# Kernel tuning notes

Hardware: AMD Instinct MI355X
Metric: run time of the kernel (lower is better)

Reference implementation:

```python
import jax, jax.numpy as jnp
import numpy as np

B = 4096
D = 512
N_I = 1000000
N_T = 1000000
GAMMA = 0.8
EPS = 1e-10
RHO_I = 8.0
RHO_T = 8.0
ETA_INIT = 1e-05
BETA_U = 0.5
GRAD_CLIP = 5.0
TAU_MIN, TAU_MAX = 0.005, 0.05
TAU_INIT = 0.01


def setup_inputs() -> dict:
    key = jax.random.key(0)
    k1, k2 = jax.random.split(key)
    img = jax.random.normal(k1, (B, D), jnp.float32)
    txt = jax.random.normal(k2, (B, D), jnp.float32)
    # CLIP-style L2-normalized features
    img = img / jnp.linalg.norm(img, axis=1, keepdims=True)
    txt = txt / jnp.linalg.norm(txt, axis=1, keepdims=True)
    return {
        "image_features": img,
        "text_features": txt,
        "s_I": jnp.zeros(N_I, jnp.float32),
        "s_T": jnp.zeros(N_T, jnp.float32),
        "b_I": jnp.zeros(N_I, jnp.float32),
        "b_T": jnp.zeros(N_T, jnp.float32),
        "u_I": jnp.zeros(N_I, jnp.float32),
        "u_T": jnp.zeros(N_T, jnp.float32),
        "tau_I": jnp.full((N_I,), TAU_INIT, jnp.float32),
        "tau_T": jnp.full((N_T,), TAU_INIT, jnp.float32),
        "image_ids": jnp.arange(B, dtype=jnp.int32),
        "text_ids": jnp.arange(B, dtype=jnp.int32),
        "epoch": 1,
    }


def reference(image_features, text_features, s_I, s_T, b_I, b_T, u_I, u_T,
              tau_I, tau_T, image_ids, text_ids, epoch):
    sg = jax.lax.stop_gradient
    sim = jnp.einsum('id,jd->ij', image_features, text_features)  # [B,B]
    diag = jnp.diagonal(sim)
    Bn = sim.shape[0]
    tau_img = tau_I[image_ids]  # [B]
    tau_txt = tau_T[text_ids]   # [B]
    image_diffs = sim - diag[:, None]
    text_diffs = sim - diag[None, :]
    # .detach() in the original -> stop_gradient here
    idt = sg(image_diffs / tau_img[:, None])
    tdt = sg(text_diffs / tau_txt[None, :])
    old_b_I = b_I[image_ids]
    old_b_T = b_T[text_ids]
    # running max for log-sum-exp stabilization
    b_I_row = jnp.maximum(idt.max(axis=1), old_b_I)
    b_T_col = jnp.maximum(tdt.max(axis=0), old_b_T)
    b_I_new = b_I.at[image_ids].set(b_I_row)
    b_T_new = b_T.at[text_ids].set(b_T_col)
    mask = 1.0 - jnp.eye(Bn, dtype=sim.dtype)
    exp_i = jnp.exp(idt - b_I_row[:, None]) * mask
    exp_t = jnp.exp(tdt - b_T_col[None, :]) * mask
    g_I = exp_i.sum(axis=1)
    g_T = exp_t.sum(axis=0)
    if epoch == 0:
        sI = g_I
        sT = g_T
    else:
        sI = (1.0 - GAMMA) * s_I[image_ids] * jnp.exp(old_b_I - b_I_row) + GAMMA * g_I
        sT = (1.0 - GAMMA) * s_T[text_ids] * jnp.exp(old_b_T - b_T_col) + GAMMA * g_T
    s_I_new = s_I.at[image_ids].set(sI)
    s_T_new = s_T.at[text_ids].set(sT)
    w_i = sg(exp_i / (sI[:, None] + EPS))
    w_t = sg(exp_t / (sT[None, :] + EPS))
    image_loss = (w_i * image_diffs).sum(axis=1)
    text_loss = (w_t * text_diffs).sum(axis=0)
    total_loss = image_loss.mean() + text_loss.mean()
    tw_i = jnp.log(sI / (Bn - 1)) + b_I_row + RHO_I - (w_i * idt).sum(axis=1)
    tw_t = jnp.log(sT / (Bn - 1)) + b_T_col + RHO_T - (w_t * tdt).sum(axis=0)
    # torch uses in-place clamp_ on a view, so the returned means are clipped
    tw_i = jnp.clip(tw_i, -GRAD_CLIP, GRAD_CLIP)
    tw_t = jnp.clip(tw_t, -GRAD_CLIP, GRAD_CLIP)
    u_I_val = (1.0 - BETA_U) * u_I[image_ids] + BETA_U * tw_i
    u_T_val = (1.0 - BETA_U) * u_T[text_ids] + BETA_U * tw_t
    u_I_new = u_I.at[image_ids].set(u_I_val)
    u_T_new = u_T.at[text_ids].set(u_T_val)
    tau_I_new = tau_I.at[image_ids].set(jnp.clip(tau_img - ETA_INIT * u_I_val, TAU_MIN, TAU_MAX))
    tau_T_new = tau_T.at[text_ids].set(jnp.clip(tau_txt - ETA_INIT * u_T_val, TAU_MIN, TAU_MAX))
    return (total_loss, tau_img.mean(), tau_txt.mean(), tw_i.mean(), tw_t.mean(),
            s_I_new, s_T_new, b_I_new, b_T_new, u_I_new, u_T_new, tau_I_new, tau_T_new)
```

## Files before the change

kernel.cpp:

```cpp
#include <hip/hip_runtime.h>

typedef unsigned short u16;
typedef unsigned int u32;

typedef __bf16 bf16x8 __attribute__((ext_vector_type(8)));
typedef float floatx4 __attribute__((ext_vector_type(4)));

__device__ __forceinline__ u16 f2bf(float f) {
    union { float f; u32 u; } c; c.f = f;
    u32 u = c.u;
    u32 r = u + 0x7FFFu + ((u >> 16) & 1u);
    return (u16)(r >> 16);
}
__device__ __forceinline__ float bf2f(u16 x) {
    union { u32 u; float f; } c; c.u = ((u32)x) << 16; return c.f;
}

__device__ __forceinline__ void comb(float& M, float& P0, float& P1,
                                     float m, float p0, float p1) {
    float nm = fmaxf(M, m);
    float s = __expf(M - nm), t = __expf(m - nm);
    P0 = P0 * s + p0 * t;
    P1 = P1 * s + p1 * t;
    M = nm;
}

__device__ __forceinline__ void gload16(const void* g, void* l) {
    __builtin_amdgcn_global_load_lds(
        (const __attribute__((address_space(1))) void*)g,
        (__attribute__((address_space(3))) void*)l, 16, 0, 0);
}

__global__ __launch_bounds__(256) void presplit(
    const float* __restrict__ a, const float* __restrict__ b,
    u16* __restrict__ Ah, u16* __restrict__ Al,
    u16* __restrict__ Bh, u16* __restrict__ Bl, int n,
    const float* __restrict__ tauI, const float* __restrict__ tauT,
    const int* __restrict__ img_ids, const int* __restrict__ txt_ids,
    float* __restrict__ taur, float* __restrict__ tauc) {
    if (blockIdx.y == 0 && blockIdx.x < 16) {
        int t = blockIdx.x * 256 + threadIdx.x;
        taur[t] = tauI[img_ids[t]];
        tauc[t] = tauT[txt_ids[t]];
    }
    const float* src = blockIdx.y ? b : a;
    u16* dh = blockIdx.y ? Bh : Ah;
    u16* dl = blockIdx.y ? Bl : Al;
    int i = (blockIdx.x * 256 + threadIdx.x) * 8;
    if (i >= n) return;
    float4 v0 = *(const float4*)&src[i];
    float4 v1 = *(const float4*)&src[i + 4];
    float xs[8] = {v0.x, v0.y, v0.z, v0.w, v1.x, v1.y, v1.z, v1.w};
    u16 h[8], l[8];
#pragma unroll
    for (int e = 0; e < 8; e++) {
        h[e] = f2bf(xs[e]);
        l[e] = f2bf(xs[e] - bf2f(h[e]));
    }
    int r = i >> 9, k = i & 511;
    int off = (((r >> 4) << 4) + (k >> 5)) * 512 + ((((k >> 3) & 3) << 4) + (r & 15)) * 8;
    *(uint4*)&dh[off] = *(uint4*)h;
    *(uint4*)&dl[off] = *(uint4*)l;
}

__global__ __launch_bounds__(512, 2) void gemm_flash(
    const u16* __restrict__ Ah, const u16* __restrict__ Al,
    const u16* __restrict__ Bh, const u16* __restrict__ Bl,
    const float* __restrict__ taur, const float* __restrict__ tauc,
    float* __restrict__ rowpart, float* __restrict__ colpart,
    float* __restrict__ diag,
    const float* __restrict__ p0, const float* __restrict__ p1,
    const float* __restrict__ p2, const float* __restrict__ p3,
    const float* __restrict__ p4, const float* __restrict__ p5,
    const float* __restrict__ p6, const float* __restrict__ p7,
    float* __restrict__ out, long long n) {
    __shared__ u16 tiles[65536];

    const int bid  = blockIdx.x;
    const int tid  = threadIdx.x;
    const int wave = tid >> 6, lane = tid & 63;
    const int lr = lane & 15, quad = lane >> 4;
    const int waveM = wave >> 2, waveN = wave & 3;
    const int x = bid & 7, s = bid >> 3;
    const int rowtile = (x >> 2) * 8 + (s >> 2);
    const int coltile = (x & 3) * 4 + (s & 3);
    const int rowBase = rowtile * 256;
    const int colBase = coltile * 256;

    const int sa = wave >> 1;
    const u16* gb = (sa == 0) ? Ah : (sa == 1) ? Al : (sa == 2) ? Bh : Bl;
    const int base16 = ((sa < 2) ? rowBase : colBase) >> 4;
    const int jb = (wave & 1) * 8;

#define STAGE(slice, bufb)                                                    \
    {                                                                         \
        _Pragma("unroll")                                                     \
        for (int j = 0; j < 8; j++) {                                         \
            size_t ge = ((size_t)(base16 + jb + j)) * 8192 +                  \
                        (size_t)(slice) * 512 + lane * 8;                     \
            gload16(gb + ge, &tiles[(bufb) + (wave * 8 + j) * 512]);          \
        }                                                                     \
    }

    floatx4 acc[8][4];
#pragma unroll
    for (int mi = 0; mi < 8; mi++)
#pragma unroll
        for (int ni = 0; ni < 4; ni++) acc[mi][ni] = (floatx4)0.0f;

    const int Gq = (int)((n - 3) >> 2);
    const int ni32 = (int)n;
    float* dst5 = out + 5;

    STAGE(0, 0)

    if (bid == 0 && tid < 32) {
        int arr = tid >> 2, j = tid & 3;
        const float* sp = (arr & 4) ? ((arr & 2) ? ((arr & 1) ? p7 : p6) : ((arr & 1) ? p5 : p4))
                                    : ((arr & 2) ? ((arr & 1) ? p3 : p2) : ((arr & 1) ? p1 : p0));
        float* dp = dst5 + (size_t)arr * (size_t)n;
        long long tail0 = 3 + 4 * (long long)Gq;
        if (j < 3) dp[j] = sp[j];
        else
            for (long long z = tail0; z < n; z++) dp[z] = sp[z];
    }
    __syncthreads();

#pragma unroll 1
    for (int t = 0; t < 16; t++) {
        const int cb = (t & 1) << 15;
        const int nb = cb ^ 32768;
        if (t < 15) STAGE(t + 1, nb)

        bool docopy = false;
        float c0 = 0.f, c1 = 0.f, c2 = 0.f, c3 = 0.f;
        int cdst = 0;
        {
            int c = bid * 512 + tid + t * 131072;
            int ck = c >> 18;
            int g = c & 262143;
            if (g < Gq) {
                docopy = true;
                int ce = 3 + 4 * g;
                cdst = ck * ni32 + ce;
                const float* sp = (ck & 4) ? ((ck & 2) ? ((ck & 1) ? p7 : p6) : ((ck & 1) ? p5 : p4))
                                           : ((ck & 2) ? ((ck & 1) ? p3 : p2) : ((ck & 1) ? p1 : p0));
                c0 = sp[ce]; c1 = sp[ce + 1]; c2 = sp[ce + 2]; c3 = sp[ce + 3];
            }
        }

        {
            const int ab = cb + lane * 8;
            bf16x8 bh[4], bl[4];
#pragma unroll
            for (int ni = 0; ni < 4; ni++) {
                bh[ni] = *(const bf16x8*)&tiles[ab + (32 + waveN * 4 + ni) * 512];
                bl[ni] = *(const bf16x8*)&tiles[ab + (48 + waveN * 4 + ni) * 512];
            }
#pragma unroll
            for (int mi = 0; mi < 8; mi++) {
                bf16x8 ah = *(const bf16x8*)&tiles[ab + (waveM * 8 + mi) * 512];
                bf16x8 al = *(const bf16x8*)&tiles[ab + (16 + waveM * 8 + mi) * 512];
#pragma unroll
                for (int ni = 0; ni < 4; ni++) {
                    acc[mi][ni] = __builtin_amdgcn_mfma_f32_16x16x32_bf16(ah, bh[ni], acc[mi][ni], 0, 0, 0);
                    acc[mi][ni] = __builtin_amdgcn_mfma_f32_16x16x32_bf16(ah, bl[ni], acc[mi][ni], 0, 0, 0);
                    acc[mi][ni] = __builtin_amdgcn_mfma_f32_16x16x32_bf16(al, bh[ni], acc[mi][ni], 0, 0, 0);
                }
            }
        }

        if (docopy) {
            float4 q = {c0, c1, c2, c3};
            *(float4*)&dst5[cdst] = q;
        }
        __syncthreads();
    }
#undef STAGE

    float* redbuf = (float*)tiles;

    if (rowtile == coltile) {
#pragma unroll
        for (int mi = 0; mi < 8; mi++)
#pragma unroll
            for (int ni = 0; ni < 4; ni++) {
                if (waveM * 128 + mi * 16 != waveN * 64 + ni * 16) continue;
#pragma unroll
                for (int r = 0; r < 4; r++)
                    if (lr == quad * 4 + r)
                        diag[colBase + waveN * 64 + ni * 16 + lr] = acc[mi][ni][r];
            }
    }

#pragma unroll
    for (int mi = 0; mi < 8; mi++) {
#pragma unroll
        for (int r = 0; r < 4; r++) {
            int row_local = waveM * 128 + mi * 16 + quad * 4 + r;
            float vmax = fmaxf(fmaxf(acc[mi][0][r], acc[mi][1][r]),
                               fmaxf(acc[mi][2][r], acc[mi][3][r]));
#pragma unroll
            for (int mask = 1; mask <= 8; mask <<= 1)
                vmax = fmaxf(vmax, __shfl_xor(vmax, mask));
            float it = 1.0f / taur[rowBase + row_local];
            float M = vmax * it;
            float P0 = 0.f, P1 = 0.f;
#pragma unroll
            for (int ni = 0; ni < 4; ni++) {
                float y = acc[mi][ni][r] * it;
                float e = __expf(y - M);
                P0 += e;
                P1 += y * e;
            }
#pragma unroll
            for (int mask = 1; mask <= 8; mask <<= 1) {
                P0 += __shfl_xor(P0, mask);
                P1 += __shfl_xor(P1, mask);
            }
            if (lr == 0) {
                int xx = (row_local * 4 + waveN) * 3;
                redbuf[xx] = M; redbuf[xx + 1] = P0; redbuf[xx + 2] = P1;
            }
        }
    }

#pragma unroll
    for (int ni = 0; ni < 4; ni++) {
        int col_local = waveN * 64 + ni * 16 + lr;
        float vmax = -3.4e38f;
#pragma unroll
        for (int mi = 0; mi < 8; mi++)
            vmax = fmaxf(vmax,
                fmaxf(fmaxf(acc[mi][ni][0], acc[mi][ni][1]),
                      fmaxf(acc[mi][ni][2], acc[mi][ni][3])));
#pragma unroll
        for (int mask = 16; mask <= 32; mask <<= 1)
            vmax = fmaxf(vmax, __shfl_xor(vmax, mask));
        float it = 1.0f / tauc[colBase + col_local];
        float M = vmax * it;
        float P0 = 0.f, P1 = 0.f;
#pragma unroll
        for (int mi = 0; mi < 8; mi++)
#pragma unroll
            for (int r = 0; r < 4; r++) {
                float y = acc[mi][ni][r] * it;
                float e = __expf(y - M);
                P0 += e;
                P1 += y * e;
            }
#pragma unroll
        for (int mask = 16; mask <= 32; mask <<= 1) {
            P0 += __shfl_xor(P0, mask);
            P1 += __shfl_xor(P1, mask);
        }
        if (quad == 0) {
            int xx = 3072 + (col_local * 2 + waveM) * 3;
            redbuf[xx] = M; redbuf[xx + 1] = P0; redbuf[xx + 2] = P1;
        }
    }
    __syncthreads();

    if (tid < 256) {
        int xx = tid * 12;
        float M = redbuf[xx], P0 = redbuf[xx + 1], P1 = redbuf[xx + 2];
        comb(M, P0, P1, redbuf[xx + 3], redbuf[xx + 4], redbuf[xx + 5]);
        comb(M, P0, P1, redbuf[xx + 6], redbuf[xx + 7], redbuf[xx + 8]);
        comb(M, P0, P1, redbuf[xx + 9], redbuf[xx + 10], redbuf[xx + 11]);
        float* dst = &rowpart[(size_t)(rowBase + tid) * 48 + coltile * 3];
        dst[0] = M; dst[1] = P0; dst[2] = P1;
    } else {
        int c = tid - 256;
        int xx = 3072 + c * 6;
        float M = redbuf[xx], P0 = redbuf[xx + 1], P1 = redbuf[xx + 2];
        comb(M, P0, P1, redbuf[xx + 3], redbuf[xx + 4], redbuf[xx + 5]);
        float* dst = &colpart[(size_t)(colBase + c) * 48 + rowtile * 3];
        dst[0] = M; dst[1] = P0; dst[2] = P1;
    }
}

struct FinArgs {
    const float* rowpart; const float* colpart; const float* diag;
    const float* tauI; const float* sI; const float* bI; const float* uI;
    const float* tauT; const float* sT; const float* bT; const float* uT;
    const int* img_ids; const int* txt_ids; const int* epoch_p;
    float* out; float* rowbuf; long long n;
};

__global__ __launch_bounds__(256) void rows_final(FinArgs a) {
    int t = blockIdx.x * 256 + threadIdx.x;
    int side = t >> 12, i = t & 4095;
    const float* part   = side ? a.colpart : a.rowpart;
    const int*   ids    = side ? a.txt_ids : a.img_ids;
    const float* tau_in = side ? a.tauT : a.tauI;
    const float* s_in   = side ? a.sT   : a.sI;
    const float* b_in   = side ? a.bT   : a.bI;
    const float* u_in   = side ? a.uT   : a.uI;

    const int id = ids[i];
    const float dg = a.diag[i];

    const float4* p4 = (const float4*)(part + (size_t)i * 48);
    float v[48];
#pragma unroll
    for (int k = 0; k < 12; k++) {
        float4 q = p4[k];
        v[4 * k]     = q.x;
        v[4 * k + 1] = q.y;
        v[4 * k + 2] = q.z;
        v[4 * k + 3] = q.w;
    }
    float M = -3.4e38f, P0 = 0.f, P1 = 0.f;
#pragma unroll
    for (int k = 0; k < 16; k++)
        comb(M, P0, P1, v[3 * k], v[3 * k + 1], v[3 * k + 2]);

    const float tau   = tau_in[id];
    const float old_b = b_in[id];
    const float old_s = s_in[id];
    const float old_u = u_in[id];
    const float y_ii  = dg / tau;

    float b_row = fmaxf(M - y_ii, old_b);
    float e  = expf(M - y_ii - b_row);
    float S0 = P0 * e - expf(-b_row);
    float S1 = (P1 - y_ii * P0) * e;

    float g = S0;
    float sI = (*a.epoch_p == 0) ? g
             : 0.2f * old_s * expf(old_b - b_row) + 0.8f * g;
    float denom = sI + 1e-10f;
    float wsum = S1 / denom;
    float lossr = tau * wsum;
    float tw = logf(sI * (1.0f / 4095.0f)) + b_row + 8.0f - wsum;
    tw = fminf(fmaxf(tw, -5.0f), 5.0f);
    float uval = 0.5f * old_u + 0.5f * tw;
    float taun = fminf(fmaxf(tau - 1e-5f * uval, 0.005f), 0.05f);

    float* sect = a.out + 5;
    sect[(size_t)(0 + side) * (size_t)a.n + id] = sI;
    sect[(size_t)(2 + side) * (size_t)a.n + id] = b_row;
    sect[(size_t)(4 + side) * (size_t)a.n + id] = uval;
    sect[(size_t)(6 + side) * (size_t)a.n + id] = taun;

    a.rowbuf[(2 * side + 0) * 4096 + i] = lossr;
    a.rowbuf[(2 * side + 1) * 4096 + i] = tw;
}

__global__ __launch_bounds__(256) void scalars(
    const float* __restrict__ rows,
    const float* __restrict__ tau_I, const float* __restrict__ tau_T,
    const int* __restrict__ image_ids, const int* __restrict__ text_ids,
    float* __restrict__ out) {
    int tid = threadIdx.x;
    int lane = tid & 63, wv = tid >> 6;
    float a[6] = {0, 0, 0, 0, 0, 0};
    for (int e = tid; e < 4096; e += 256) {
        a[0] += rows[0 * 4096 + e];
        a[1] += rows[1 * 4096 + e];
        a[2] += rows[2 * 4096 + e];
        a[3] += rows[3 * 4096 + e];
        a[4] += tau_I[image_ids[e]];
        a[5] += tau_T[text_ids[e]];
    }
    __shared__ float sred[4][6];
#pragma unroll
    for (int k = 0; k < 6; k++)
        for (int o = 32; o > 0; o >>= 1) a[k] += __shfl_xor(a[k], o);
    if (lane == 0)
#pragma unroll
        for (int k = 0; k < 6; k++) sred[wv][k] = a[k];
    __syncthreads();
    if (tid == 0) {
#pragma unroll
        for (int k = 0; k < 6; k++)
            a[k] = sred[0][k] + sred[1][k] + sred[2][k] + sred[3][k];
        const float inv = 1.0f / 4096.0f;
        out[0] = (a[0] + a[2]) * inv;
        out[1] = a[4] * inv;
        out[2] = a[5] * inv;
        out[3] = a[1] * inv;
        out[4] = a[3] * inv;
    }
}

extern "C" void kernel_launch(void* const* d_in, const int* in_sizes, int n_in,
                              void* d_out, int out_size, void* d_ws, size_t ws_size,
                              hipStream_t stream) {
    const float* img   = (const float*)d_in[0];
    const float* txt   = (const float*)d_in[1];
    const float* s_I   = (const float*)d_in[2];
    const float* s_T   = (const float*)d_in[3];
    const float* b_I   = (const float*)d_in[4];
    const float* b_T   = (const float*)d_in[5];
    const float* u_I   = (const float*)d_in[6];
    const float* u_T   = (const float*)d_in[7];
    const float* tau_I = (const float*)d_in[8];
    const float* tau_T = (const float*)d_in[9];
    const int* image_ids = (const int*)d_in[10];
    const int* text_ids  = (const int*)d_in[11];
    const int* epoch     = (const int*)d_in[12];
    float* out = (float*)d_out;
    const long long n = in_sizes[2];
    const int nfeat = in_sizes[0];

    const size_t MB = 1024 * 1024;
    u16* Ah = (u16*)d_ws;
    u16* Al = Ah + (size_t)nfeat;
    u16* Bh = Al + (size_t)nfeat;
    u16* Bl = Bh + (size_t)nfeat;
    float* rowpart = (float*)((char*)d_ws + 16 * MB);
    float* colpart = (float*)((char*)d_ws + 18 * MB);
    float* diag    = (float*)((char*)d_ws + 20 * MB);
    float* taur    = (float*)((char*)d_ws + 20 * MB + 256 * 1024);
    float* tauc    = (float*)((char*)d_ws + 20 * MB + 512 * 1024);
    float* rows    = (float*)((char*)d_ws + 21 * MB);

    presplit<<<dim3((nfeat / 8 + 255) / 256, 2), 256, 0, stream>>>(
        img, txt, Ah, Al, Bh, Bl, nfeat,
        tau_I, tau_T, image_ids, text_ids, taur, tauc);

    gemm_flash<<<256, 512, 0, stream>>>(
        Ah, Al, Bh, Bl, taur, tauc, rowpart, colpart, diag,
        s_I, s_T, b_I, b_T, u_I, u_T, tau_I, tau_T, out, n);

    FinArgs fa;
    fa.rowpart = rowpart; fa.colpart = colpart; fa.diag = diag;
    fa.tauI = tau_I; fa.sI = s_I; fa.bI = b_I; fa.uI = u_I;
    fa.tauT = tau_T; fa.sT = s_T; fa.bT = b_T; fa.uT = u_T;
    fa.img_ids = image_ids; fa.txt_ids = text_ids; fa.epoch_p = epoch;
    fa.out = out; fa.rowbuf = rows; fa.n = n;
    rows_final<<<32, 256, 0, stream>>>(fa);

    scalars<<<1, 256, 0, stream>>>(rows, tau_I, tau_T, image_ids, text_ids, out);
}
```

Before: 178.3 us.

## Split LDS staging into hi/lo halves with a two-deep prefetch and finer barriers

Each K-slice is now staged as separate hi and lo halves, with two slices prefetched ahead. The single per-iteration syncthreads is replaced by explicit vmcnt/lgkmcnt waits and s_barriers. The three MFMA passes (hi*hi, lo*hi, hi*lo) are split into phases so the next slice's global-to-LDS loads can be issued after each half is consumed, and s_setprio is raised around MFMA bursts. The aim is to overlap global loads with compute more deeply and cut barrier stalls. It adds register pressure (ah[8] kept live across phases), and the hand-written waitcnt counts are a correctness risk.

```diff
diff --git a/kernel.cpp b/kernel.cpp
--- a/kernel.cpp
+++ b/kernel.cpp
@@ -30,6 +30,8 @@
         (const __attribute__((address_space(1))) void*)g,
         (__attribute__((address_space(3))) void*)l, 16, 0, 0);
 }
+
+#define MEMFENCE() asm volatile("" ::: "memory")
 
 __global__ __launch_bounds__(256) void presplit(
     const float* __restrict__ a, const float* __restrict__ b,
@@ -61,6 +63,22 @@
     int off = (((r >> 4) << 4) + (k >> 5)) * 512 + ((((k >> 3) & 3) << 4) + (r & 15)) * 8;
     *(uint4*)&dh[off] = *(uint4*)h;
     *(uint4*)&dl[off] = *(uint4*)l;
+}
+
+__device__ __forceinline__ void stage_half(
+    const u16* __restrict__ X, const u16* __restrict__ Y,
+    int rowBase16, int colBase16, int slice, int wave, int lane,
+    u16* lds_slot) {
+#pragma unroll
+    for (int j = 0; j < 4; j++) {
+        int gf = wave * 4 + j;
+        const u16* src;
+        size_t ge;
+        if (gf < 16) { src = X; ge = ((size_t)(rowBase16 + gf)) * 8192; }
+        else         { src = Y; ge = ((size_t)(colBase16 + gf - 16)) * 8192; }
+        ge += (size_t)slice * 512 + (size_t)(lane * 8);
+        gload16(src + ge, lds_slot + gf * 512);
+    }
 }
 
 __global__ __launch_bounds__(512, 2) void gemm_flash(
@@ -86,21 +104,8 @@
     const int coltile = (x & 3) * 4 + (s & 3);
     const int rowBase = rowtile * 256;
     const int colBase = coltile * 256;
-
-    const int sa = wave >> 1;
-    const u16* gb = (sa == 0) ? Ah : (sa == 1) ? Al : (sa == 2) ? Bh : Bl;
-    const int base16 = ((sa < 2) ? rowBase : colBase) >> 4;
-    const int jb = (wave & 1) * 8;
-
-#define STAGE(slice, bufb)                                                    \
-    {                                                                         \
-        _Pragma("unroll")                                                     \
-        for (int j = 0; j < 8; j++) {                                         \
-            size_t ge = ((size_t)(base16 + jb + j)) * 8192 +                  \
-                        (size_t)(slice) * 512 + lane * 8;                     \
-            gload16(gb + ge, &tiles[(bufb) + (wave * 8 + j) * 512]);          \
-        }                                                                     \
-    }
+    const int rowBase16 = rowBase >> 4, colBase16 = colBase >> 4;
+    const int la = lane * 8;
 
     floatx4 acc[8][4];
 #pragma unroll
@@ -111,8 +116,6 @@
     const int Gq = (int)((n - 3) >> 2);
     const int ni32 = (int)n;
     float* dst5 = out + 5;
-
-    STAGE(0, 0)
 
     if (bid == 0 && tid < 32) {
         int arr = tid >> 2, j = tid & 3;
@@ -124,13 +127,21 @@
         else
             for (long long z = tail0; z < n; z++) dp[z] = sp[z];
     }
-    __syncthreads();
+
+    stage_half(Ah, Bh, rowBase16, colBase16, 0, wave, lane, tiles);
+    stage_half(Al, Bl, rowBase16, colBase16, 0, wave, lane, tiles + 16384);
+    stage_half(Ah, Bh, rowBase16, colBase16, 1, wave, lane, tiles + 32768);
+    stage_half(Al, Bl, rowBase16, colBase16, 1, wave, lane, tiles + 49152);
 
 #pragma unroll 1
     for (int t = 0; t < 16; t++) {
-        const int cb = (t & 1) << 15;
-        const int nb = cb ^ 32768;
-        if (t < 15) STAGE(t + 1, nb)
+        const int s0 = (t & 1) << 15;
+        const int s1 = s0 + 16384;
+
+        if (t == 15) { asm volatile("s_waitcnt vmcnt(0)" ::: "memory"); }
+        else         { asm volatile("s_waitcnt vmcnt(8)" ::: "memory"); }
+        __builtin_amdgcn_s_barrier();
+        MEMFENCE();
 
         bool docopy = false;
         float c0 = 0.f, c1 = 0.f, c2 = 0.f, c3 = 0.f;
@@ -149,34 +160,64 @@
             }
         }
 
-        {
-            const int ab = cb + lane * 8;
-            bf16x8 bh[4], bl[4];
-#pragma unroll
-            for (int ni = 0; ni < 4; ni++) {
-                bh[ni] = *(const bf16x8*)&tiles[ab + (32 + waveN * 4 + ni) * 512];
-                bl[ni] = *(const bf16x8*)&tiles[ab + (48 + waveN * 4 + ni) * 512];
-            }
-#pragma unroll
-            for (int mi = 0; mi < 8; mi++) {
-                bf16x8 ah = *(const bf16x8*)&tiles[ab + (waveM * 8 + mi) * 512];
-                bf16x8 al = *(const bf16x8*)&tiles[ab + (16 + waveM * 8 + mi) * 512];
-#pragma unroll
-                for (int ni = 0; ni < 4; ni++) {
-                    acc[mi][ni] = __builtin_amdgcn_mfma_f32_16x16x32_bf16(ah, bh[ni], acc[mi][ni], 0, 0, 0);
-                    acc[mi][ni] = __builtin_amdgcn_mfma_f32_16x16x32_bf16(ah, bl[ni], acc[mi][ni], 0, 0, 0);
-                    acc[mi][ni] = __builtin_amdgcn_mfma_f32_16x16x32_bf16(al, bh[ni], acc[mi][ni], 0, 0, 0);
-                }
-            }
-        }
+        bf16x8 ah[8], bh[4], bl[4];
+#pragma unroll
+        for (int ni = 0; ni < 4; ni++)
+            bh[ni] = *(const bf16x8*)&tiles[s0 + (16 + waveN * 4 + ni) * 512 + la];
+#pragma unroll
+        for (int mi = 0; mi < 8; mi++)
+            ah[mi] = *(const bf16x8*)&tiles[s0 + (waveM * 8 + mi) * 512 + la];
+        asm volatile("s_waitcnt lgkmcnt(0)" ::: "memory");
+        __builtin_amdgcn_sched_barrier(0);
+        __builtin_amdgcn_s_setprio(1);
+#pragma unroll
+        for (int mi = 0; mi < 8; mi++)
+#pragma unroll
+            for (int ni = 0; ni < 4; ni++)
+                acc[mi][ni] = __builtin_amdgcn_mfma_f32_16x16x32_bf16(ah[mi], bh[ni], acc[mi][ni], 0, 0, 0);
+        __builtin_amdgcn_s_setprio(0);
+        MEMFENCE();
+        __builtin_amdgcn_s_barrier();
+        MEMFENCE();
+
+        if (t < 14)
+            stage_half(Ah, Bh, rowBase16, colBase16, t + 2, wave, lane,
+                       tiles + (s0 >> 0));
+#pragma unroll
+        for (int ni = 0; ni < 4; ni++)
+            bl[ni] = *(const bf16x8*)&tiles[s1 + (16 + waveN * 4 + ni) * 512 + la];
+        __builtin_amdgcn_s_setprio(1);
+#pragma unroll
+        for (int mi = 0; mi < 8; mi++) {
+            bf16x8 al = *(const bf16x8*)&tiles[s1 + (waveM * 8 + mi) * 512 + la];
+#pragma unroll
+            for (int ni = 0; ni < 4; ni++)
+                acc[mi][ni] = __builtin_amdgcn_mfma_f32_16x16x32_bf16(al, bh[ni], acc[mi][ni], 0, 0, 0);
+        }
+        __builtin_amdgcn_s_setprio(0);
+        asm volatile("s_waitcnt lgkmcnt(0)" ::: "memory");
+        MEMFENCE();
+        __builtin_amdgcn_s_barrier();
+        MEMFENCE();
+
+        if (t < 14)
+            stage_half(Al, Bl, rowBase16, colBase16, t + 2, wave, lane,
+                       tiles + (s1 >> 0));
+        __builtin_amdgcn_s_setprio(1);
+#pragma unroll
+        for (int mi = 0; mi < 8; mi++)
+#pragma unroll
+            for (int ni = 0; ni < 4; ni++)
+                acc[mi][ni] = __builtin_amdgcn_mfma_f32_16x16x32_bf16(ah[mi], bl[ni], acc[mi][ni], 0, 0, 0);
+        __builtin_amdgcn_s_setprio(0);
 
         if (docopy) {
             float4 q = {c0, c1, c2, c3};
             *(float4*)&dst5[cdst] = q;
         }
-        __syncthreads();
-    }
-#undef STAGE
+    }
+
+    __syncthreads();
 
     float* redbuf = (float*)tiles;
 
```

Result: slower. 211.4 us (+18.6%).

## Interleave LDS reads, MFMA clusters and staged global loads with explicit barriers

Applied to the files above, without the earlier changes.

The main k-loop is restructured into six phases. Each phase loads a subset of A/B fragments from LDS, issues a quarter of the next slice's global-to-LDS loads, waits with lgkmcnt(0), and runs a 16-MFMA cluster at raised wave priority, with s_barrier between phases. The aim is to spread global prefetch across the compute instead of issuing it all at once, and to keep MFMA issue dense through ping-pong style scheduling. The risk is extra barriers and a vmcnt(0) wait each iteration, which could add stalls. Register pressure also rises from holding more fragments.

```diff
diff --git a/kernel.cpp b/kernel.cpp
--- a/kernel.cpp
+++ b/kernel.cpp
@@ -30,6 +30,11 @@
         (const __attribute__((address_space(1))) void*)g,
         (__attribute__((address_space(3))) void*)l, 16, 0, 0);
 }
+
+#define BARRIER() asm volatile("s_barrier" ::: "memory")
+#define LGKM0()                                            \
+    asm volatile("s_waitcnt lgkmcnt(0)" ::: "memory");     \
+    __builtin_amdgcn_sched_barrier(0)
 
 __global__ __launch_bounds__(256) void presplit(
     const float* __restrict__ a, const float* __restrict__ b,
@@ -86,19 +91,22 @@
     const int coltile = (x & 3) * 4 + (s & 3);
     const int rowBase = rowtile * 256;
     const int colBase = coltile * 256;
+    const int rowBase16 = rowBase >> 4, colBase16 = colBase >> 4;
+    const int la = lane * 8;
 
     const int sa = wave >> 1;
     const u16* gb = (sa == 0) ? Ah : (sa == 1) ? Al : (sa == 2) ? Bh : Bl;
-    const int base16 = ((sa < 2) ? rowBase : colBase) >> 4;
+    const int base16 = (sa < 2) ? rowBase16 : colBase16;
     const int jb = (wave & 1) * 8;
-
-#define STAGE(slice, bufb)                                                    \
+    const int fb = sa * 16 + jb;
+
+#define STAGE2(slice, nbuf, j0)                                               \
     {                                                                         \
         _Pragma("unroll")                                                     \
-        for (int j = 0; j < 8; j++) {                                         \
+        for (int j = (j0); j < (j0) + 2; j++) {                               \
             size_t ge = ((size_t)(base16 + jb + j)) * 8192 +                  \
-                        (size_t)(slice) * 512 + lane * 8;                     \
-            gload16(gb + ge, &tiles[(bufb) + (wave * 8 + j) * 512]);          \
+                        (size_t)(slice) * 512 + (size_t)la;                   \
+            gload16(gb + ge, (nbuf) + (fb + j) * 512);                        \
         }                                                                     \
     }
 
@@ -111,8 +119,6 @@
     const int Gq = (int)((n - 3) >> 2);
     const int ni32 = (int)n;
     float* dst5 = out + 5;
-
-    STAGE(0, 0)
 
     if (bid == 0 && tid < 32) {
         int arr = tid >> 2, j = tid & 3;
@@ -124,13 +130,16 @@
         else
             for (long long z = tail0; z < n; z++) dp[z] = sp[z];
     }
+
+    STAGE2(0, tiles, 0) STAGE2(0, tiles, 2) STAGE2(0, tiles, 4) STAGE2(0, tiles, 6)
+    asm volatile("s_waitcnt vmcnt(0)" ::: "memory");
     __syncthreads();
 
 #pragma unroll 1
     for (int t = 0; t < 16; t++) {
         const int cb = (t & 1) << 15;
-        const int nb = cb ^ 32768;
-        if (t < 15) STAGE(t + 1, nb)
+        u16* nbuf = tiles + (cb ^ 32768);
+        const int ab = cb + la;
 
         bool docopy = false;
         float c0 = 0.f, c1 = 0.f, c2 = 0.f, c3 = 0.f;
@@ -149,34 +158,102 @@
             }
         }
 
-        {
-            const int ab = cb + lane * 8;
-            bf16x8 bh[4], bl[4];
-#pragma unroll
-            for (int ni = 0; ni < 4; ni++) {
-                bh[ni] = *(const bf16x8*)&tiles[ab + (32 + waveN * 4 + ni) * 512];
-                bl[ni] = *(const bf16x8*)&tiles[ab + (48 + waveN * 4 + ni) * 512];
-            }
-#pragma unroll
-            for (int mi = 0; mi < 8; mi++) {
-                bf16x8 ah = *(const bf16x8*)&tiles[ab + (waveM * 8 + mi) * 512];
-                bf16x8 al = *(const bf16x8*)&tiles[ab + (16 + waveM * 8 + mi) * 512];
-#pragma unroll
-                for (int ni = 0; ni < 4; ni++) {
-                    acc[mi][ni] = __builtin_amdgcn_mfma_f32_16x16x32_bf16(ah, bh[ni], acc[mi][ni], 0, 0, 0);
-                    acc[mi][ni] = __builtin_amdgcn_mfma_f32_16x16x32_bf16(ah, bl[ni], acc[mi][ni], 0, 0, 0);
-                    acc[mi][ni] = __builtin_amdgcn_mfma_f32_16x16x32_bf16(al, bh[ni], acc[mi][ni], 0, 0, 0);
-                }
-            }
-        }
-
+        bf16x8 ah[8], bh[4], bl[4], al[4];
+
+#pragma unroll
+        for (int k = 0; k < 4; k++)
+            bh[k] = *(const bf16x8*)&tiles[ab + (32 + waveN * 4 + k) * 512];
+#pragma unroll
+        for (int k = 0; k < 4; k++)
+            ah[k] = *(const bf16x8*)&tiles[ab + (waveM * 8 + k) * 512];
+        if (t < 15) STAGE2(t + 1, nbuf, 0)
+        BARRIER();
+        LGKM0();
+        __builtin_amdgcn_s_setprio(1);
+#pragma unroll
+        for (int mi = 0; mi < 4; mi++)
+#pragma unroll
+            for (int ni = 0; ni < 4; ni++)
+                acc[mi][ni] = __builtin_amdgcn_mfma_f32_16x16x32_bf16(ah[mi], bh[ni], acc[mi][ni], 0, 0, 0);
+        __builtin_amdgcn_s_setprio(0);
+        BARRIER();
+
+#pragma unroll
+        for (int k = 0; k < 4; k++)
+            ah[4 + k] = *(const bf16x8*)&tiles[ab + (waveM * 8 + 4 + k) * 512];
+        if (t < 15) STAGE2(t + 1, nbuf, 2)
+        BARRIER();
+        LGKM0();
+        __builtin_amdgcn_s_setprio(1);
+#pragma unroll
+        for (int mi = 4; mi < 8; mi++)
+#pragma unroll
+            for (int ni = 0; ni < 4; ni++)
+                acc[mi][ni] = __builtin_amdgcn_mfma_f32_16x16x32_bf16(ah[mi], bh[ni], acc[mi][ni], 0, 0, 0);
+        __builtin_amdgcn_s_setprio(0);
+        BARRIER();
+
+#pragma unroll
+        for (int k = 0; k < 4; k++)
+            al[k] = *(const bf16x8*)&tiles[ab + (16 + waveM * 8 + k) * 512];
+        if (t < 15) STAGE2(t + 1, nbuf, 4)
+        BARRIER();
+        LGKM0();
+        __builtin_amdgcn_s_setprio(1);
+#pragma unroll
+        for (int mi = 0; mi < 4; mi++)
+#pragma unroll
+            for (int ni = 0; ni < 4; ni++)
+                acc[mi][ni] = __builtin_amdgcn_mfma_f32_16x16x32_bf16(al[mi], bh[ni], acc[mi][ni], 0, 0, 0);
+        __builtin_amdgcn_s_setprio(0);
+        BARRIER();
+
+#pragma unroll
+        for (int k = 0; k < 4; k++)
+            al[k] = *(const bf16x8*)&tiles[ab + (16 + waveM * 8 + 4 + k) * 512];
+        if (t < 15) STAGE2(t + 1, nbuf, 6)
+        BARRIER();
+        LGKM0();
+        __builtin_amdgcn_s_setprio(1);
+#pragma unroll
+        for (int mi = 0; mi < 4; mi++)
+#pragma unroll
+            for (int ni = 0; ni < 4; ni++)
+                acc[4 + mi][ni] = __builtin_amdgcn_mfma_f32_16x16x32_bf16(al[mi], bh[ni], acc[4 + mi][ni], 0, 0, 0);
+        __builtin_amdgcn_s_setprio(0);
+        BARRIER();
+
+#pragma unroll
+        for (int k = 0; k < 4; k++)
+            bl[k] = *(const bf16x8*)&tiles[ab + (48 + waveN * 4 + k) * 512];
+        BARRIER();
+        LGKM0();
+        __builtin_amdgcn_s_setprio(1);
+#pragma unroll
+        for (int mi = 0; mi < 4; mi++)
+#pragma unroll
+            for (int ni = 0; ni < 4; ni++)
+                acc[mi][ni] = __builtin_amdgcn_mfma_f32_16x16x32_bf16(ah[mi], bl[ni], acc[mi][ni], 0, 0, 0);
+        __builtin_amdgcn_s_setprio(0);
+        BARRIER();
+
+        __builtin_amdgcn_s_setprio(1);
+#pragma unroll
+        for (int mi = 4; mi < 8; mi++)
+#pragma unroll
+            for (int ni = 0; ni < 4; ni++)
+                acc[mi][ni] = __builtin_amdgcn_mfma_f32_16x16x32_bf16(ah[mi], bl[ni], acc[mi][ni], 0, 0, 0);
+        __builtin_amdgcn_s_setprio(0);
+        asm volatile("s_waitcnt vmcnt(0)" ::: "memory");
         if (docopy) {
             float4 q = {c0, c1, c2, c3};
             *(float4*)&dst5[cdst] = q;
         }
-        __syncthreads();
-    }
-#undef STAGE
+        BARRIER();
+    }
+#undef STAGE2
+
+    __syncthreads();
 
     float* redbuf = (float*)tiles;
 
```

Result: no change. 180.5 us (+1.2%).

## Fuse row finalization and scalar reduction into GEMM kernel via grid barrier

Applied to the files above, without the earlier changes.

Removes the separate rows_final and scalars launches. After writing partials, every GEMM block increments an atomic counter, and the first 16 blocks spin until all 256 have arrived before running the per-row finalization. Block sums are accumulated with float atomics, and the last-arriving block writes the scalar outputs. This cuts two kernel launches and their launch gaps, but it depends on all 256 blocks being co-resident for the spin barrier and makes the float reduction order nondeterministic.

```diff
diff --git a/kernel.cpp b/kernel.cpp
--- a/kernel.cpp
+++ b/kernel.cpp
@@ -37,7 +37,10 @@
     u16* __restrict__ Bh, u16* __restrict__ Bl, int n,
     const float* __restrict__ tauI, const float* __restrict__ tauT,
     const int* __restrict__ img_ids, const int* __restrict__ txt_ids,
-    float* __restrict__ taur, float* __restrict__ tauc) {
+    float* __restrict__ taur, float* __restrict__ tauc,
+    u32* __restrict__ ctrl) {
+    if (blockIdx.y == 0 && blockIdx.x == 0 && threadIdx.x < 8)
+        ctrl[threadIdx.x] = 0u;
     if (blockIdx.y == 0 && blockIdx.x < 16) {
         int t = blockIdx.x * 256 + threadIdx.x;
         taur[t] = tauI[img_ids[t]];
@@ -73,7 +76,9 @@
     const float* __restrict__ p2, const float* __restrict__ p3,
     const float* __restrict__ p4, const float* __restrict__ p5,
     const float* __restrict__ p6, const float* __restrict__ p7,
-    float* __restrict__ out, long long n) {
+    float* __restrict__ out, long long n,
+    const int* __restrict__ img_ids, const int* __restrict__ txt_ids,
+    const int* __restrict__ epoch_p, u32* __restrict__ ctrl) {
     __shared__ u16 tiles[65536];
 
     const int bid  = blockIdx.x;
@@ -277,110 +282,121 @@
         float* dst = &colpart[(size_t)(colBase + c) * 48 + rowtile * 3];
         dst[0] = M; dst[1] = P0; dst[2] = P1;
     }
-}
-
-struct FinArgs {
-    const float* rowpart; const float* colpart; const float* diag;
-    const float* tauI; const float* sI; const float* bI; const float* uI;
-    const float* tauT; const float* sT; const float* bT; const float* uT;
-    const int* img_ids; const int* txt_ids; const int* epoch_p;
-    float* out; float* rowbuf; long long n;
-};
-
-__global__ __launch_bounds__(256) void rows_final(FinArgs a) {
-    int t = blockIdx.x * 256 + threadIdx.x;
-    int side = t >> 12, i = t & 4095;
-    const float* part   = side ? a.colpart : a.rowpart;
-    const int*   ids    = side ? a.txt_ids : a.img_ids;
-    const float* tau_in = side ? a.tauT : a.tauI;
-    const float* s_in   = side ? a.sT   : a.sI;
-    const float* b_in   = side ? a.bT   : a.bI;
-    const float* u_in   = side ? a.uT   : a.uI;
-
-    const int id = ids[i];
-    const float dg = a.diag[i];
-
-    const float4* p4 = (const float4*)(part + (size_t)i * 48);
-    float v[48];
-#pragma unroll
-    for (int k = 0; k < 12; k++) {
-        float4 q = p4[k];
-        v[4 * k]     = q.x;
-        v[4 * k + 1] = q.y;
-        v[4 * k + 2] = q.z;
-        v[4 * k + 3] = q.w;
-    }
-    float M = -3.4e38f, P0 = 0.f, P1 = 0.f;
-#pragma unroll
-    for (int k = 0; k < 16; k++)
-        comb(M, P0, P1, v[3 * k], v[3 * k + 1], v[3 * k + 2]);
-
-    const float tau   = tau_in[id];
-    const float old_b = b_in[id];
-    const float old_s = s_in[id];
-    const float old_u = u_in[id];
-    const float y_ii  = dg / tau;
-
-    float b_row = fmaxf(M - y_ii, old_b);
-    float e  = expf(M - y_ii - b_row);
-    float S0 = P0 * e - expf(-b_row);
-    float S1 = (P1 - y_ii * P0) * e;
-
-    float g = S0;
-    float sI = (*a.epoch_p == 0) ? g
-             : 0.2f * old_s * expf(old_b - b_row) + 0.8f * g;
-    float denom = sI + 1e-10f;
-    float wsum = S1 / denom;
-    float lossr = tau * wsum;
-    float tw = logf(sI * (1.0f / 4095.0f)) + b_row + 8.0f - wsum;
-    tw = fminf(fmaxf(tw, -5.0f), 5.0f);
-    float uval = 0.5f * old_u + 0.5f * tw;
-    float taun = fminf(fmaxf(tau - 1e-5f * uval, 0.005f), 0.05f);
-
-    float* sect = a.out + 5;
-    sect[(size_t)(0 + side) * (size_t)a.n + id] = sI;
-    sect[(size_t)(2 + side) * (size_t)a.n + id] = b_row;
-    sect[(size_t)(4 + side) * (size_t)a.n + id] = uval;
-    sect[(size_t)(6 + side) * (size_t)a.n + id] = taun;
-
-    a.rowbuf[(2 * side + 0) * 4096 + i] = lossr;
-    a.rowbuf[(2 * side + 1) * 4096 + i] = tw;
-}
-
-__global__ __launch_bounds__(256) void scalars(
-    const float* __restrict__ rows,
-    const float* __restrict__ tau_I, const float* __restrict__ tau_T,
-    const int* __restrict__ image_ids, const int* __restrict__ text_ids,
-    float* __restrict__ out) {
-    int tid = threadIdx.x;
-    int lane = tid & 63, wv = tid >> 6;
-    float a[6] = {0, 0, 0, 0, 0, 0};
-    for (int e = tid; e < 4096; e += 256) {
-        a[0] += rows[0 * 4096 + e];
-        a[1] += rows[1 * 4096 + e];
-        a[2] += rows[2 * 4096 + e];
-        a[3] += rows[3 * 4096 + e];
-        a[4] += tau_I[image_ids[e]];
-        a[5] += tau_T[text_ids[e]];
-    }
-    __shared__ float sred[4][6];
-#pragma unroll
-    for (int k = 0; k < 6; k++)
-        for (int o = 32; o > 0; o >>= 1) a[k] += __shfl_xor(a[k], o);
-    if (lane == 0)
-#pragma unroll
-        for (int k = 0; k < 6; k++) sred[wv][k] = a[k];
+
+    __threadfence();
+    if (tid == 0)
+        __hip_atomic_fetch_add(&ctrl[0], 1u, __ATOMIC_RELEASE,
+                               __HIP_MEMORY_SCOPE_AGENT);
+    if (bid >= 16) return;
+
+    if (tid == 0) {
+        while (__hip_atomic_load(&ctrl[0], __ATOMIC_ACQUIRE,
+                                 __HIP_MEMORY_SCOPE_AGENT) < 256u)
+            __builtin_amdgcn_s_sleep(2);
+    }
     __syncthreads();
-    if (tid == 0) {
-#pragma unroll
-        for (int k = 0; k < 6; k++)
-            a[k] = sred[0][k] + sred[1][k] + sred[2][k] + sred[3][k];
-        const float inv = 1.0f / 4096.0f;
-        out[0] = (a[0] + a[2]) * inv;
-        out[1] = a[4] * inv;
-        out[2] = a[5] * inv;
-        out[3] = a[1] * inv;
-        out[4] = a[3] * inv;
+    (void)__hip_atomic_load(&ctrl[0], __ATOMIC_ACQUIRE, __HIP_MEMORY_SCOPE_AGENT);
+
+    {
+        const int t = bid * 512 + tid;
+        const int side = t >> 12, i = t & 4095;
+        const float* part = side ? colpart : rowpart;
+        const int*   ids  = side ? txt_ids : img_ids;
+        const float* s_in = side ? p1 : p0;
+        const float* b_in = side ? p3 : p2;
+        const float* u_in = side ? p5 : p4;
+
+        const int id = ids[i];
+        const float dg  = diag[i];
+        const float tau = side ? tauc[i] : taur[i];
+
+        const float4* pq = (const float4*)(part + (size_t)i * 48);
+        float v[48];
+#pragma unroll
+        for (int k = 0; k < 12; k++) {
+            float4 q = pq[k];
+            v[4 * k] = q.x; v[4 * k + 1] = q.y;
+            v[4 * k + 2] = q.z; v[4 * k + 3] = q.w;
+        }
+        float M = -3.4e38f, P0 = 0.f, P1 = 0.f;
+#pragma unroll
+        for (int k = 0; k < 16; k++)
+            comb(M, P0, P1, v[3 * k], v[3 * k + 1], v[3 * k + 2]);
+
+        const float old_b = b_in[id];
+        const float old_s = s_in[id];
+        const float old_u = u_in[id];
+        const float y_ii  = dg / tau;
+
+        float b_row = fmaxf(M - y_ii, old_b);
+        float e  = expf(M - y_ii - b_row);
+        float S0 = P0 * e - expf(-b_row);
+        float S1 = (P1 - y_ii * P0) * e;
+
+        float g = S0;
+        float sI = (*epoch_p == 0) ? g
+                 : 0.2f * old_s * expf(old_b - b_row) + 0.8f * g;
+        float denom = sI + 1e-10f;
+        float wsum = S1 / denom;
+        float lossr = tau * wsum;
+        float tw = logf(sI * (1.0f / 4095.0f)) + b_row + 8.0f - wsum;
+        tw = fminf(fmaxf(tw, -5.0f), 5.0f);
+        float uval = 0.5f * old_u + 0.5f * tw;
+        float taun = fminf(fmaxf(tau - 1e-5f * uval, 0.005f), 0.05f);
+
+        float* sect = out + 5;
+        sect[(size_t)(0 + side) * (size_t)n + id] = sI;
+        sect[(size_t)(2 + side) * (size_t)n + id] = b_row;
+        sect[(size_t)(4 + side) * (size_t)n + id] = uval;
+        sect[(size_t)(6 + side) * (size_t)n + id] = taun;
+
+        float r0 = lossr, r1 = tw, r2 = tau;
+#pragma unroll
+        for (int o = 32; o > 0; o >>= 1) {
+            r0 += __shfl_xor(r0, o);
+            r1 += __shfl_xor(r1, o);
+            r2 += __shfl_xor(r2, o);
+        }
+        __syncthreads();
+        if (lane == 0) {
+            redbuf[wave * 3 + 0] = r0;
+            redbuf[wave * 3 + 1] = r1;
+            redbuf[wave * 3 + 2] = r2;
+        }
+        __syncthreads();
+        if (tid == 0) {
+            float t0 = 0.f, t1 = 0.f, t2 = 0.f;
+#pragma unroll
+            for (int w = 0; w < 8; w++) {
+                t0 += redbuf[w * 3 + 0];
+                t1 += redbuf[w * 3 + 1];
+                t2 += redbuf[w * 3 + 2];
+            }
+            float* accs = (float*)(ctrl + 2);
+            __hip_atomic_fetch_add(&accs[side * 3 + 0], t0, __ATOMIC_RELAXED,
+                                   __HIP_MEMORY_SCOPE_AGENT);
+            __hip_atomic_fetch_add(&accs[side * 3 + 1], t1, __ATOMIC_RELAXED,
+                                   __HIP_MEMORY_SCOPE_AGENT);
+            __hip_atomic_fetch_add(&accs[side * 3 + 2], t2, __ATOMIC_RELAXED,
+                                   __HIP_MEMORY_SCOPE_AGENT);
+            __threadfence();
+            u32 tk = __hip_atomic_fetch_add(&ctrl[1], 1u, __ATOMIC_ACQ_REL,
+                                            __HIP_MEMORY_SCOPE_AGENT);
+            if (tk == 15u) {
+                float a0 = __hip_atomic_load(&accs[0], __ATOMIC_ACQUIRE, __HIP_MEMORY_SCOPE_AGENT);
+                float a1 = __hip_atomic_load(&accs[1], __ATOMIC_ACQUIRE, __HIP_MEMORY_SCOPE_AGENT);
+                float a2 = __hip_atomic_load(&accs[2], __ATOMIC_ACQUIRE, __HIP_MEMORY_SCOPE_AGENT);
+                float a3 = __hip_atomic_load(&accs[3], __ATOMIC_ACQUIRE, __HIP_MEMORY_SCOPE_AGENT);
+                float a4 = __hip_atomic_load(&accs[4], __ATOMIC_ACQUIRE, __HIP_MEMORY_SCOPE_AGENT);
+                float a5 = __hip_atomic_load(&accs[5], __ATOMIC_ACQUIRE, __HIP_MEMORY_SCOPE_AGENT);
+                const float inv = 1.0f / 4096.0f;
+                out[0] = (a0 + a3) * inv;
+                out[1] = a2 * inv;
+                out[2] = a5 * inv;
+                out[3] = a1 * inv;
+                out[4] = a4 * inv;
+            }
+        }
     }
 }
 
@@ -414,23 +430,14 @@
     float* diag    = (float*)((char*)d_ws + 20 * MB);
     float* taur    = (float*)((char*)d_ws + 20 * MB + 256 * 1024);
     float* tauc    = (float*)((char*)d_ws + 20 * MB + 512 * 1024);
-    float* rows    = (float*)((char*)d_ws + 21 * MB);
+    u32*   ctrl    = (u32*)((char*)d_ws + 22 * MB);
 
     presplit<<<dim3((nfeat / 8 + 255) / 256, 2), 256, 0, stream>>>(
         img, txt, Ah, Al, Bh, Bl, nfeat,
-        tau_I, tau_T, image_ids, text_ids, taur, tauc);
+        tau_I, tau_T, image_ids, text_ids, taur, tauc, ctrl);
 
     gemm_flash<<<256, 512, 0, stream>>>(
         Ah, Al, Bh, Bl, taur, tauc, rowpart, colpart, diag,
-        s_I, s_T, b_I, b_T, u_I, u_T, tau_I, tau_T, out, n);
-
-    FinArgs fa;
-    fa.rowpart = rowpart; fa.colpart = colpart; fa.diag = diag;
-    fa.tauI = tau_I; fa.sI = s_I; fa.bI = b_I; fa.uI = u_I;
-    fa.tauT = tau_T; fa.sT = s_T; fa.bT = b_T; fa.uT = u_T;
-    fa.img_ids = image_ids; fa.txt_ids = text_ids; fa.epoch_p = epoch;
-    fa.out = out; fa.rowbuf = rows; fa.n = n;
-    rows_final<<<32, 256, 0, stream>>>(fa);
-
-    scalars<<<1, 256, 0, stream>>>(rows, tau_I, tau_T, image_ids, text_ids, out);
-}
+        s_I, s_T, b_I, b_T, u_I, u_T, tau_I, tau_T, out, n,
+        image_ids, text_ids, epoch, ctrl);
+}
```

New measurement: 238.9 us. 34.0% more time.
